# Kernel tuning notes

Measured on AMD Instinct MI355X. Metric: run time of the kernel, lower is better.

## Reference

```python
import jax, jax.numpy as jnp
import numpy as np

INV_TEMP = 20.0
THRESHOLD = 0.01
EPS = 1e-12


def setup_inputs() -> dict:
    key = jax.random.key(0)
    k1, k2, k3, k4, k5 = jax.random.split(key, 5)
    B, NA, NB, D, K = 1, 4096, 4096, 256, 8
    return {
        "keypoints_A": jax.random.uniform(k1, (B, NA, 2), jnp.float32) * 2.0 - 1.0,
        "descriptions_A": jax.random.normal(k2, (B, NA, D), jnp.float32),
        "keypoints_B": jax.random.uniform(k3, (B, NB, 2), jnp.float32) * 2.0 - 1.0,
        "descriptions_B": jax.random.normal(k4, (B, NB, D), jnp.float32),
        # steerer prototype affine maps: one DxD matrix per prototype, scaled to
        # keep steered descriptors at unit-ish norm (acts like ~orthogonal map)
        "prototype_mats": jax.random.normal(k5, (K, D, D), jnp.float32) / np.float32(np.sqrt(D)),
    }


def _neg_dist_similarity(a, b):
    # negative Euclidean distance, matching -torch.cdist(a, b)
    a2 = jnp.sum(a * a, axis=-1)[..., :, None]   # [B, NA, 1]
    b2 = jnp.sum(b * b, axis=-1)[..., None, :]   # [B, 1, NB]
    d2 = jnp.maximum(a2 + b2 - 2.0 * jnp.einsum('bnd,bmd->bnm', a, b), 0.0)
    return -jnp.sqrt(d2 + EPS)                   # [B, NA, NB]


def reference(keypoints_A, descriptions_A, keypoints_B, descriptions_B, prototype_mats):
    # base similarity
    corr = _neg_dist_similarity(descriptions_A, descriptions_B)  # [B, NA, NB]

    # looped augmented-similarity max-accumulate (one pass per prototype affine)
    def step(c, M):
        dA_aug = jnp.einsum('bnd,ed->bne', descriptions_A, M)  # steered descriptors
        return jnp.maximum(c, _neg_dist_similarity(dA_aug, descriptions_B)), None

    corr, _ = jax.lax.scan(step, corr, prototype_mats)

    corr = INV_TEMP * corr
    # dual softmax matching
    P = jax.nn.softmax(corr, axis=-2) * jax.nn.softmax(corr, axis=-1)  # [B, NA, NB]

    # mutual nearest neighbour + threshold (fixed-shape boolean mask instead of nonzero)
    mask = (P == P.max(axis=-1, keepdims=True)) \
         & (P == P.max(axis=-2, keepdims=True)) \
         & (P > THRESHOLD)

    # fixed-shape match extraction: best B-index per A keypoint + validity flag
    j = jnp.argmax(P, axis=-1)                                   # [B, NA]
    valid = jnp.take_along_axis(mask, j[..., None], axis=-1)[..., 0]  # [B, NA]
    matches_B = jnp.take_along_axis(keypoints_B, j[..., None], axis=1)  # [B, NA, 2]
    return P, mask, valid, matches_B
```

## Files before the change

### kernel.cpp

```cpp
#include <hip/hip_runtime.h>
#include <math.h>

#define NPT 4096
#define DIM 256
#define NVAR 9
#define INV_TEMP 20.0f
#define THR 0.01f
#define EPSD 1e-12f

typedef unsigned short u16;
typedef __attribute__((ext_vector_type(8))) __bf16 bf16x8;
typedef __attribute__((ext_vector_type(4))) float f32x4;

__device__ __forceinline__ unsigned frep(float x) {
    unsigned u = __float_as_uint(x);
    return (u & 0x80000000u) ? ~u : (u | 0x80000000u);
}
__device__ __forceinline__ float funrep(unsigned u) {
    return __uint_as_float((u & 0x80000000u) ? (u ^ 0x80000000u) : ~u);
}

__device__ __forceinline__ u16 f2bf(float x) {
    unsigned u = __float_as_uint(x);
    u += 0x7fffu + ((u >> 16) & 1u);
    return (u16)(u >> 16);
}
__device__ __forceinline__ float bf2f(u16 h) {
    return __uint_as_float(((unsigned)h) << 16);
}
__device__ __forceinline__ void split_hl(float x, u16& h, u16& l) {
    u16 hh = f2bf(x);
    h = hh;
    l = f2bf(x - bf2f(hh));
}

__device__ __forceinline__ void gl_lds16(const void* g, void* l) {
    __builtin_amdgcn_global_load_lds(
        (const __attribute__((address_space(1))) void*)g,
        (__attribute__((address_space(3))) void*)l, 16, 0, 0);
}

#define NA4 (NPT * DIM / 4)
#define NP4 (8 * DIM * DIM / 4)
__global__ __launch_bounds__(256) void conv3_kernel(const float* __restrict__ A,
                                                    const float* __restrict__ B,
                                                    const float* __restrict__ Pr,
                                                    u16* __restrict__ Ahi, u16* __restrict__ Alo,
                                                    u16* __restrict__ Bhi, u16* __restrict__ Blo,
                                                    u16* __restrict__ Phi, u16* __restrict__ Plo) {
    int i = blockIdx.x * 256 + threadIdx.x;
    const float* src;
    u16 *dh, *dl;
    int j;
    if (i < NA4) { src = A; dh = Ahi; dl = Alo; j = i; }
    else if (i < 2 * NA4) { src = B; dh = Bhi; dl = Blo; j = i - NA4; }
    else if (i < 2 * NA4 + NP4) { src = Pr; dh = Phi; dl = Plo; j = i - 2 * NA4; }
    else return;
    float4 v = ((const float4*)src)[j];
    ushort4 h, l;
    split_hl(v.x, h.x, l.x);
    split_hl(v.y, h.y, l.y);
    split_hl(v.z, h.z, l.z);
    split_hl(v.w, h.w, l.w);
    ((ushort4*)dh)[j] = h;
    ((ushort4*)dl)[j] = l;
}

__global__ __launch_bounds__(256, 2) void steer_mfma_kernel(
    const u16* __restrict__ A0h, const u16* __restrict__ A0l,
    const u16* __restrict__ Ph, const u16* __restrict__ Pl,
    u16* __restrict__ outH, u16* __restrict__ outL,
    float* __restrict__ a2out) {
    __shared__ u16 lds[32768];
    u16* LAh = lds;
    u16* LAl = lds + 8192;
    u16* LBh = lds + 16384;
    u16* LBl = lds + 24576;

    const int tid = threadIdx.x, lane = tid & 63, wave = tid >> 6;
    const int l15 = lane & 15, lg = lane >> 4;
    const int wr = (wave >> 1) * 64, wc = (wave & 1) * 64;
    const int rb = blockIdx.x * 128;
    const int eb = blockIdx.y * 128;
    const int k = blockIdx.z;
    const u16* Bh_g = Ph + (size_t)k * DIM * DIM;
    const u16* Bl_g = Pl + (size_t)k * DIM * DIM;
    const int s_row = tid >> 3;
    const int s_ch = tid & 7;
    const int s_gch = s_ch ^ (s_row & 7);
    const int c0 = lg ^ (l15 & 7);

    f32x4 acc[4][4];
#pragma unroll
    for (int m = 0; m < 4; ++m)
#pragma unroll
        for (int n = 0; n < 4; ++n) acc[m][n] = 0.0f;

    for (int kb = 0; kb < 4; ++kb) {
        const int k0 = kb * 64;
        __syncthreads();
#pragma unroll
        for (int r = 0; r < 4; ++r) {
            int row = r * 32 + s_row;
            size_t ga = (size_t)(rb + row) * DIM + k0 + s_gch * 8;
            size_t gb = (size_t)(eb + row) * DIM + k0 + s_gch * 8;
            int lo = row * 64 + s_ch * 8;
            gl_lds16(A0h + ga, &LAh[lo]);
            gl_lds16(A0l + ga, &LAl[lo]);
            gl_lds16(Bh_g + gb, &LBh[lo]);
            gl_lds16(Bl_g + gb, &LBl[lo]);
        }
        __syncthreads();
#pragma unroll
        for (int ks = 0; ks < 2; ++ks) {
            const int cx = (c0 ^ (ks << 2)) * 8;
            bf16x8 ah[4], al[4], bh[4], bl[4];
#pragma unroll
            for (int m = 0; m < 4; ++m) {
                int ro = (wr + m * 16 + l15) * 64 + cx;
                ah[m] = *(const bf16x8*)&LAh[ro];
                al[m] = *(const bf16x8*)&LAl[ro];
            }
#pragma unroll
            for (int n = 0; n < 4; ++n) {
                int ro = (wc + n * 16 + l15) * 64 + cx;
                bh[n] = *(const bf16x8*)&LBh[ro];
                bl[n] = *(const bf16x8*)&LBl[ro];
            }
#pragma unroll
            for (int m = 0; m < 4; ++m)
#pragma unroll
                for (int n = 0; n < 4; ++n)
                    acc[m][n] = __builtin_amdgcn_mfma_f32_16x16x32_bf16(ah[m], bh[n], acc[m][n], 0, 0, 0);
#pragma unroll
            for (int m = 0; m < 4; ++m)
#pragma unroll
                for (int n = 0; n < 4; ++n)
                    acc[m][n] = __builtin_amdgcn_mfma_f32_16x16x32_bf16(al[m], bh[n], acc[m][n], 0, 0, 0);
#pragma unroll
            for (int m = 0; m < 4; ++m)
#pragma unroll
                for (int n = 0; n < 4; ++n)
                    acc[m][n] = __builtin_amdgcn_mfma_f32_16x16x32_bf16(ah[m], bl[n], acc[m][n], 0, 0, 0);
        }
    }
#pragma unroll
    for (int m = 0; m < 4; ++m)
#pragma unroll
        for (int j = 0; j < 4; ++j) {
            size_t row = (size_t)(k + 1) * NPT + rb + wr + m * 16 + lg * 4 + j;
            float s2 = 0.f;
#pragma unroll
            for (int n = 0; n < 4; ++n) {
                float s = acc[m][n][j];
                s2 += s * s;
                u16 h, l;
                split_hl(s, h, l);
                size_t idx = row * DIM + eb + wc + n * 16 + l15;
                outH[idx] = h;
                outL[idx] = l;
            }
            s2 += __shfl_xor(s2, 1);
            s2 += __shfl_xor(s2, 2);
            s2 += __shfl_xor(s2, 4);
            s2 += __shfl_xor(s2, 8);
            if (l15 == 0) atomicAdd(&a2out[row], s2);
        }
}

__global__ __launch_bounds__(256) void rownorm2_kernel(const u16* __restrict__ AH,
                                                       const u16* __restrict__ AL,
                                                       const u16* __restrict__ BH,
                                                       const u16* __restrict__ BL,
                                                       float* __restrict__ out) {
    int w = blockIdx.x * 4 + (threadIdx.x >> 6);
    int lane = threadIdx.x & 63;
    const u16 *H, *L;
    size_t row;
    int oidx;
    if (w < NPT) { H = AH; L = AL; row = w; oidx = w; }
    else { H = BH; L = BL; row = w - NPT; oidx = NVAR * NPT + (w - NPT); }
    ushort4 h = *(const ushort4*)&H[row * DIM + lane * 4];
    ushort4 l = *(const ushort4*)&L[row * DIM + lane * 4];
    float x0 = bf2f(h.x) + bf2f(l.x);
    float x1 = bf2f(h.y) + bf2f(l.y);
    float x2 = bf2f(h.z) + bf2f(l.z);
    float x3 = bf2f(h.w) + bf2f(l.w);
    float s = x0 * x0 + x1 * x1 + x2 * x2 + x3 * x3;
#pragma unroll
    for (int o = 32; o; o >>= 1) s += __shfl_xor(s, o);
    if (lane == 0) out[oidx] = s;
}

__global__ __launch_bounds__(256, 2) void corr_mfma_kernel(
    const u16* __restrict__ Ahi, const u16* __restrict__ Alo,
    const u16* __restrict__ Bhi, const u16* __restrict__ Blo,
    const float* __restrict__ a2, const float* __restrict__ b2,
    float* __restrict__ cOut, unsigned* __restrict__ rm_rep, unsigned* __restrict__ cm_rep,
    float* __restrict__ pMaxR, float* __restrict__ pSumR,
    float* __restrict__ pMaxC, float* __restrict__ pSumC) {
    __shared__ u16 lds[32768];
    u16* LAh = lds;
    u16* LAl = lds + 8192;
    u16* LBh = lds + 16384;
    u16* LBl = lds + 24576;

    const int tid = threadIdx.x, lane = tid & 63, wave = tid >> 6;
    const int l15 = lane & 15, lg = lane >> 4;
    const int wr = (wave >> 1) * 64, wc = (wave & 1) * 64;
    int wg = blockIdx.y * 32 + blockIdx.x;
    const int xcd = wg & 7, idx8 = wg >> 3;
    const int rbIdx = ((xcd >> 1) << 3) + (idx8 >> 4);
    const int cbIdx = ((xcd & 1) << 4) + (idx8 & 15);
    const int rb = rbIdx << 7;
    const int cb = cbIdx << 7;
    const int s_row = tid >> 3;
    const int s_ch = tid & 7;
    const int s_gch = s_ch ^ (s_row & 7);
    const int c0 = lg ^ (l15 & 7);

    float b2c[4];
#pragma unroll
    for (int n = 0; n < 4; ++n) b2c[n] = b2[cb + wc + n * 16 + l15];

    f32x4 zmin[4][4];
#pragma unroll
    for (int m = 0; m < 4; ++m)
#pragma unroll
        for (int n = 0; n < 4; ++n) zmin[m][n] = 3.402823466e38f;

    for (int v = 0; v < NVAR; ++v) {
        const u16* Ah_g = Ahi + (size_t)v * NPT * DIM;
        const u16* Al_g = Alo + (size_t)v * NPT * DIM;
        f32x4 acc[4][4];
#pragma unroll
        for (int m = 0; m < 4; ++m)
#pragma unroll
            for (int n = 0; n < 4; ++n) acc[m][n] = 0.0f;

        for (int kb = 0; kb < 4; ++kb) {
            const int k0 = kb * 64;
            __syncthreads();
#pragma unroll
            for (int r = 0; r < 4; ++r) {
                int row = r * 32 + s_row;
                size_t ga = (size_t)(rb + row) * DIM + k0 + s_gch * 8;
                size_t gb = (size_t)(cb + row) * DIM + k0 + s_gch * 8;
                int lo = row * 64 + s_ch * 8;
                gl_lds16(Ah_g + ga, &LAh[lo]);
                gl_lds16(Al_g + ga, &LAl[lo]);
                gl_lds16(Bhi + gb, &LBh[lo]);
                gl_lds16(Blo + gb, &LBl[lo]);
            }
            __syncthreads();
#pragma unroll
            for (int ks = 0; ks < 2; ++ks) {
                const int cx = (c0 ^ (ks << 2)) * 8;
                bf16x8 ah[4], al[4], bh[4], bl[4];
#pragma unroll
                for (int m = 0; m < 4; ++m) {
                    int ro = (wr + m * 16 + l15) * 64 + cx;
                    ah[m] = *(const bf16x8*)&LAh[ro];
                    al[m] = *(const bf16x8*)&LAl[ro];
                }
#pragma unroll
                for (int n = 0; n < 4; ++n) {
                    int ro = (wc + n * 16 + l15) * 64 + cx;
                    bh[n] = *(const bf16x8*)&LBh[ro];
                    bl[n] = *(const bf16x8*)&LBl[ro];
                }
#pragma unroll
                for (int m = 0; m < 4; ++m)
#pragma unroll
                    for (int n = 0; n < 4; ++n)
                        acc[m][n] = __builtin_amdgcn_mfma_f32_16x16x32_bf16(ah[m], bh[n], acc[m][n], 0, 0, 0);
#pragma unroll
                for (int m = 0; m < 4; ++m)
#pragma unroll
                    for (int n = 0; n < 4; ++n)
                        acc[m][n] = __builtin_amdgcn_mfma_f32_16x16x32_bf16(al[m], bh[n], acc[m][n], 0, 0, 0);
#pragma unroll
                for (int m = 0; m < 4; ++m)
#pragma unroll
                    for (int n = 0; n < 4; ++n)
                        acc[m][n] = __builtin_amdgcn_mfma_f32_16x16x32_bf16(ah[m], bl[n], acc[m][n], 0, 0, 0);
            }
        }
#pragma unroll
        for (int m = 0; m < 4; ++m) {
            float4 a4 = *(const float4*)&a2[(size_t)v * NPT + rb + wr + m * 16 + lg * 4];
            const float* a4p = (const float*)&a4;
#pragma unroll
            for (int n = 0; n < 4; ++n)
#pragma unroll
                for (int j = 0; j < 4; ++j) {
                    float d2 = fmaxf(a4p[j] + b2c[n] - 2.0f * acc[m][n][j], 0.0f);
                    zmin[m][n][j] = fminf(zmin[m][n][j], d2);
                }
        }
    }

    unsigned* redR = (unsigned*)lds;
    unsigned* redC = redR + 128;
    float* bsumR = (float*)(redC + 128);
    float* bsumC = bsumR + 128;
    __syncthreads();
    if (tid < 128) { redR[tid] = 0u; redC[tid] = 0u; bsumR[tid] = 0.f; bsumC[tid] = 0.f; }
    __syncthreads();

    float colmax[4] = {-3.402823466e38f, -3.402823466e38f, -3.402823466e38f, -3.402823466e38f};
#pragma unroll
    for (int m = 0; m < 4; ++m) {
#pragma unroll
        for (int j = 0; j < 4; ++j) {
            int row = rb + wr + m * 16 + lg * 4 + j;
            float rmax = -3.402823466e38f;
#pragma unroll
            for (int n = 0; n < 4; ++n) {
                float c = -INV_TEMP * sqrtf(zmin[m][n][j] + EPSD);
                cOut[(size_t)row * NPT + cb + wc + n * 16 + l15] = c;
                rmax = fmaxf(rmax, c);
                colmax[n] = fmaxf(colmax[n], c);
            }
            atomicMax(&redR[wr + m * 16 + lg * 4 + j], frep(rmax));
        }
    }
#pragma unroll
    for (int n = 0; n < 4; ++n)
        atomicMax(&redC[wc + n * 16 + l15], frep(colmax[n]));
    __syncthreads();

    float bmc[4], colS[4];
#pragma unroll
    for (int n = 0; n < 4; ++n) {
        bmc[n] = funrep(redC[wc + n * 16 + l15]);
        colS[n] = 0.f;
    }
#pragma unroll
    for (int m = 0; m < 4; ++m) {
#pragma unroll
        for (int j = 0; j < 4; ++j) {
            int lr = wr + m * 16 + lg * 4 + j;
            float bm = funrep(redR[lr]);
            float s = 0.f;
#pragma unroll
            for (int n = 0; n < 4; ++n) {
                float c = -INV_TEMP * sqrtf(zmin[m][n][j] + EPSD);
                s += __expf(c - bm);
                colS[n] += __expf(c - bmc[n]);
            }
            s += __shfl_xor(s, 1);
            s += __shfl_xor(s, 2);
            s += __shfl_xor(s, 4);
            s += __shfl_xor(s, 8);
            if (l15 == 0) atomicAdd(&bsumR[lr], s);
        }
    }
#pragma unroll
    for (int n = 0; n < 4; ++n) {
        float s = colS[n];
        s += __shfl_xor(s, 16);
        s += __shfl_xor(s, 32);
        if (lg == 0) atomicAdd(&bsumC[wc + n * 16 + l15], s);
    }
    __syncthreads();

    if (tid < 128) {
        atomicMax(&rm_rep[rb + tid], redR[tid]);
        pMaxR[(size_t)cbIdx * NPT + rb + tid] = funrep(redR[tid]);
        pSumR[(size_t)cbIdx * NPT + rb + tid] = bsumR[tid];
    } else {
        int t = tid - 128;
        atomicMax(&cm_rep[cb + t], redC[t]);
        pMaxC[(size_t)rbIdx * NPT + cb + t] = funrep(redC[t]);
        pSumC[(size_t)rbIdx * NPT + cb + t] = bsumC[t];
    }
}

__global__ __launch_bounds__(256) void combine_kernel(const unsigned* __restrict__ rm_rep,
                                                      const unsigned* __restrict__ cm_rep,
                                                      const float* __restrict__ pMaxR,
                                                      const float* __restrict__ pSumR,
                                                      const float* __restrict__ pMaxC,
                                                      const float* __restrict__ pSumC,
                                                      float* __restrict__ rowsum,
                                                      float* __restrict__ colsum) {
    int idx = (blockIdx.x & 15) * 256 + threadIdx.x;
    if (blockIdx.x < 16) {
        float gm = funrep(rm_rep[idx]);
        float s = 0.f;
#pragma unroll
        for (int b = 0; b < 32; ++b)
            s += pSumR[(size_t)b * NPT + idx] * __expf(pMaxR[(size_t)b * NPT + idx] - gm);
        rowsum[idx] = s;
    } else {
        float gm = funrep(cm_rep[idx]);
        float s = 0.f;
#pragma unroll
        for (int b = 0; b < 32; ++b)
            s += pSumC[(size_t)b * NPT + idx] * __expf(pMaxC[(size_t)b * NPT + idx] - gm);
        colsum[idx] = s;
    }
}


__global__ __launch_bounds__(256) void pmax_kernel(float* __restrict__ C,
                                                   const unsigned* __restrict__ rm_rep,
                                                   const unsigned* __restrict__ cm_rep,
                                                   const float* __restrict__ rowsum,
                                                   const float* __restrict__ colsum,
                                                   unsigned* __restrict__ rmp_rep,
                                                   unsigned* __restrict__ cmp_rep) {
    const int tid = threadIdx.x, lane = tid & 63, wv = tid >> 6;
    const int c0 = (blockIdx.x & 15) * 256;
    const int r0 = (blockIdx.x >> 4) * 64;
    const int colq = (c0 >> 2) + lane;
    __shared__ float rmbuf[64], rrbuf[64];
    __shared__ float pmLds[64 * 65];
    __shared__ float qred[256];
    __shared__ float cred[4][256];
    if (tid < 64) {
        rmbuf[tid] = funrep(rm_rep[r0 + tid]);
        rrbuf[tid] = 1.0f / rowsum[r0 + tid];
    }
    uint4 cmr = ((const uint4*)cm_rep)[colq];
    float cm0 = funrep(cmr.x), cm1 = funrep(cmr.y), cm2 = funrep(cmr.z), cm3 = funrep(cmr.w);
    float4 csv = ((const float4*)colsum)[colq];
    float rc0 = 1.0f / csv.x, rc1 = 1.0f / csv.y, rc2 = 1.0f / csv.z, rc3 = 1.0f / csv.w;
    __syncthreads();
    float4 cmax = make_float4(-1.f, -1.f, -1.f, -1.f);
#pragma unroll
    for (int it = 0; it < 16; ++it) {
        int lr = it * 4 + wv;
        int r = r0 + lr;
        size_t idx = (size_t)r * (NPT / 4) + colq;
        float4 cv = ((const float4*)C)[idx];
        float rm = rmbuf[lr];
        float rr = rrbuf[lr];
        float4 p;
        p.x = __expf(2.0f * cv.x - cm0 - rm) * (rc0 * rr);
        p.y = __expf(2.0f * cv.y - cm1 - rm) * (rc1 * rr);
        p.z = __expf(2.0f * cv.z - cm2 - rm) * (rc2 * rr);
        p.w = __expf(2.0f * cv.w - cm3 - rm) * (rc3 * rr);
        ((float4*)C)[idx] = p;
        pmLds[lr * 65 + lane] = fmaxf(fmaxf(p.x, p.y), fmaxf(p.z, p.w));
        cmax.x = fmaxf(cmax.x, p.x);
        cmax.y = fmaxf(cmax.y, p.y);
        cmax.z = fmaxf(cmax.z, p.z);
        cmax.w = fmaxf(cmax.w, p.w);
    }
    cred[wv][lane * 4 + 0] = cmax.x;
    cred[wv][lane * 4 + 1] = cmax.y;
    cred[wv][lane * 4 + 2] = cmax.z;
    cred[wv][lane * 4 + 3] = cmax.w;
    __syncthreads();
    {
        int row = tid & 63, q = tid >> 6;
        float m = -1.f;
#pragma unroll
        for (int i = 0; i < 16; ++i) m = fmaxf(m, pmLds[row * 65 + q * 16 + i]);
        qred[row * 4 + q] = m;
    }
    float mc = fmaxf(fmaxf(cred[0][tid], cred[1][tid]), fmaxf(cred[2][tid], cred[3][tid]));
    atomicMax(&cmp_rep[c0 + tid], frep(mc));
    __syncthreads();
    if (tid < 64) {
        float m = fmaxf(fmaxf(qred[tid * 4 + 0], qred[tid * 4 + 1]),
                        fmaxf(qred[tid * 4 + 2], qred[tid * 4 + 3]));
        atomicMax(&rmp_rep[r0 + tid], frep(m));
    }
}

__global__ __launch_bounds__(256) void maskarg_kernel(const float* __restrict__ P,
                                                      const unsigned* __restrict__ rmp_rep,
                                                      const unsigned* __restrict__ cmp_rep,
                                                      float* __restrict__ maskOut,
                                                      int* __restrict__ argJ) {
    const int tid = threadIdx.x, lane = tid & 63, wv = tid >> 6;
    const int c0 = (blockIdx.x & 15) * 256;
    const int r0 = (blockIdx.x >> 4) * 64;
    const int colq = (c0 >> 2) + lane;
    const int col4 = c0 + lane * 4;
    __shared__ float rpbuf[64];
    __shared__ int candLds[64 * 65];
    __shared__ int qredi[256];
    if (tid < 64) rpbuf[tid] = funrep(rmp_rep[r0 + tid]);
    uint4 cpr = ((const uint4*)cmp_rep)[colq];
    float cp0 = funrep(cpr.x), cp1 = funrep(cpr.y), cp2 = funrep(cpr.z), cp3 = funrep(cpr.w);
    __syncthreads();
#pragma unroll
    for (int it = 0; it < 16; ++it) {
        int lr = it * 4 + wv;
        int r = r0 + lr;
        size_t idx = (size_t)r * (NPT / 4) + colq;
        float4 p = ((const float4*)P)[idx];
        float rmp = rpbuf[lr];
        float4 m;
        m.x = (p.x == rmp && p.x == cp0 && p.x > THR) ? 1.f : 0.f;
        m.y = (p.y == rmp && p.y == cp1 && p.y > THR) ? 1.f : 0.f;
        m.z = (p.z == rmp && p.z == cp2 && p.z > THR) ? 1.f : 0.f;
        m.w = (p.w == rmp && p.w == cp3 && p.w > THR) ? 1.f : 0.f;
        ((float4*)maskOut)[idx] = m;
        int cand = 0x7fffffff;
        if (p.w == rmp) cand = col4 + 3;
        if (p.z == rmp) cand = col4 + 2;
        if (p.y == rmp) cand = col4 + 1;
        if (p.x == rmp) cand = col4 + 0;
        candLds[lr * 65 + lane] = cand;
    }
    __syncthreads();
    {
        int row = tid & 63, q = tid >> 6;
        int m = 0x7fffffff;
#pragma unroll
        for (int i = 0; i < 16; ++i) m = min(m, candLds[row * 65 + q * 16 + i]);
        qredi[row * 4 + q] = m;
    }
    __syncthreads();
    if (tid < 64) {
        int m = min(min(qredi[tid * 4 + 0], qredi[tid * 4 + 1]),
                    min(qredi[tid * 4 + 2], qredi[tid * 4 + 3]));
        atomicMin(&argJ[r0 + tid], m);
    }
}

__global__ __launch_bounds__(256) void valid_kernel(const float* __restrict__ P,
                                                    const unsigned* __restrict__ cmp_rep,
                                                    const int* __restrict__ argJ,
                                                    const float* __restrict__ kpB,
                                                    float* __restrict__ validOut,
                                                    float* __restrict__ matchOut) {
    int n = blockIdx.x * 256 + threadIdx.x;
    int j = argJ[n];
    float pj = P[(size_t)n * NPT + j];
    bool v = (pj == funrep(cmp_rep[j])) && (pj > THR);
    validOut[n] = v ? 1.f : 0.f;
    matchOut[2 * n + 0] = kpB[2 * j + 0];
    matchOut[2 * n + 1] = kpB[2 * j + 1];
}

extern "C" void kernel_launch(void* const* d_in, const int* in_sizes, int n_in,
                              void* d_out, int out_size, void* d_ws, size_t ws_size,
                              hipStream_t stream) {
    const float* dA     = (const float*)d_in[1];
    const float* kpB    = (const float*)d_in[2];
    const float* dB     = (const float*)d_in[3];
    const float* protos = (const float*)d_in[4];

    float* P      = (float*)d_out;
    float* maskO  = P + (size_t)NPT * NPT;
    float* validO = maskO + (size_t)NPT * NPT;
    float* matchO = validO + NPT;

    u16* Ahi = (u16*)maskO;
    u16* Alo = Ahi + (size_t)NVAR * NPT * DIM;
    u16* Bhi = Alo + (size_t)NVAR * NPT * DIM;
    u16* Blo = Bhi + (size_t)NPT * DIM;
    u16* Phi = Blo + (size_t)NPT * DIM;
    u16* Plo = Phi + (size_t)8 * DIM * DIM;
    float* pMaxR = (float*)(Plo + (size_t)8 * DIM * DIM);
    float* pSumR = pMaxR + 32 * NPT;
    float* pMaxC = pSumR + 32 * NPT;
    float* pSumC = pMaxC + 32 * NPT;

    float* ws      = (float*)d_ws;
    float* a2      = ws;
    float* b2      = a2 + NVAR * NPT;
    unsigned* rm   = (unsigned*)(b2 + NPT);
    unsigned* cm   = rm + NPT;
    unsigned* rmp  = cm + NPT;
    unsigned* cmp  = rmp + NPT;
    float* rs      = (float*)(cmp + NPT);
    float* cs      = rs + NPT;
    int* argJ      = (int*)(cs + NPT);

    hipMemsetAsync(a2 + NPT, 0, 8 * NPT * sizeof(float), stream);
    hipMemsetAsync(rm, 0, 4 * NPT * sizeof(unsigned), stream);
    hipMemsetAsync(argJ, 0x7f, NPT * sizeof(int), stream);

    conv3_kernel<<<2560, 256, 0, stream>>>(dA, dB, protos, Ahi, Alo, Bhi, Blo, Phi, Plo);
    steer_mfma_kernel<<<dim3(32, 2, 8), 256, 0, stream>>>(Ahi, Alo, Phi, Plo, Ahi, Alo, a2);
    rownorm2_kernel<<<2 * NPT / 4, 256, 0, stream>>>(Ahi, Alo, Bhi, Blo, a2);
    corr_mfma_kernel<<<dim3(32, 32), 256, 0, stream>>>(Ahi, Alo, Bhi, Blo, a2, b2, P, rm, cm,
                                                       pMaxR, pSumR, pMaxC, pSumC);
    combine_kernel<<<32, 256, 0, stream>>>(rm, cm, pMaxR, pSumR, pMaxC, pSumC, rs, cs);
    pmax_kernel<<<1024, 256, 0, stream>>>(P, rm, cm, rs, cs, rmp, cmp);
    maskarg_kernel<<<1024, 256, 0, stream>>>(P, rmp, cmp, maskO, argJ);
    valid_kernel<<<16, 256, 0, stream>>>(P, cmp, argJ, kpB, validO, matchO);
}
```

Measured before the change: 424.6 us.

## Double-buffer corr GEMM LDS loads and fuse row norms into conversion

The corr kernel's K loop changes from 64-wide single-buffered tiles with two barriers per step to 32-wide double-buffered tiles. The next tile is issued into the alternate LDS buffer while MFMAs run on the current one, which hides global-load latency and leaves one barrier per step. The XOR swizzle is dropped, so LDS bank conflicts may rise. Separately, the A and B row squared norms are now computed inside the conversion kernel, which removes the rownorm2 launch and its re-read of the split data.

Measured after the change: 507.0 us. 19.4% more time.

```diff
diff --git a/kernel.cpp b/kernel.cpp
--- a/kernel.cpp
+++ b/kernel.cpp
@@ -47,13 +47,16 @@
                                                     const float* __restrict__ Pr,
                                                     u16* __restrict__ Ahi, u16* __restrict__ Alo,
                                                     u16* __restrict__ Bhi, u16* __restrict__ Blo,
-                                                    u16* __restrict__ Phi, u16* __restrict__ Plo) {
+                                                    u16* __restrict__ Phi, u16* __restrict__ Plo,
+                                                    float* __restrict__ a2,
+                                                    float* __restrict__ b2) {
     int i = blockIdx.x * 256 + threadIdx.x;
     const float* src;
     u16 *dh, *dl;
     int j;
-    if (i < NA4) { src = A; dh = Ahi; dl = Alo; j = i; }
-    else if (i < 2 * NA4) { src = B; dh = Bhi; dl = Blo; j = i - NA4; }
+    bool isA = false, isB = false;
+    if (i < NA4) { src = A; dh = Ahi; dl = Alo; j = i; isA = true; }
+    else if (i < 2 * NA4) { src = B; dh = Bhi; dl = Blo; j = i - NA4; isB = true; }
     else if (i < 2 * NA4 + NP4) { src = Pr; dh = Phi; dl = Plo; j = i - 2 * NA4; }
     else return;
     float4 v = ((const float4*)src)[j];
@@ -64,6 +67,20 @@
     split_hl(v.w, h.w, l.w);
     ((ushort4*)dh)[j] = h;
     ((ushort4*)dl)[j] = l;
+    if (isA || isB) {
+        float x0 = bf2f(h.x) + bf2f(l.x);
+        float x1 = bf2f(h.y) + bf2f(l.y);
+        float x2 = bf2f(h.z) + bf2f(l.z);
+        float x3 = bf2f(h.w) + bf2f(l.w);
+        float s = x0 * x0 + x1 * x1 + x2 * x2 + x3 * x3;
+#pragma unroll
+        for (int o = 32; o; o >>= 1) s += __shfl_xor(s, o);
+        if ((threadIdx.x & 63) == 0) {
+            int row = j >> 6;
+            if (isA) a2[row] = s;
+            else b2[row] = s;
+        }
+    }
 }
 
 __global__ __launch_bounds__(256, 2) void steer_mfma_kernel(
@@ -168,30 +185,6 @@
         }
 }
 
-__global__ __launch_bounds__(256) void rownorm2_kernel(const u16* __restrict__ AH,
-                                                       const u16* __restrict__ AL,
-                                                       const u16* __restrict__ BH,
-                                                       const u16* __restrict__ BL,
-                                                       float* __restrict__ out) {
-    int w = blockIdx.x * 4 + (threadIdx.x >> 6);
-    int lane = threadIdx.x & 63;
-    const u16 *H, *L;
-    size_t row;
-    int oidx;
-    if (w < NPT) { H = AH; L = AL; row = w; oidx = w; }
-    else { H = BH; L = BL; row = w - NPT; oidx = NVAR * NPT + (w - NPT); }
-    ushort4 h = *(const ushort4*)&H[row * DIM + lane * 4];
-    ushort4 l = *(const ushort4*)&L[row * DIM + lane * 4];
-    float x0 = bf2f(h.x) + bf2f(l.x);
-    float x1 = bf2f(h.y) + bf2f(l.y);
-    float x2 = bf2f(h.z) + bf2f(l.z);
-    float x3 = bf2f(h.w) + bf2f(l.w);
-    float s = x0 * x0 + x1 * x1 + x2 * x2 + x3 * x3;
-#pragma unroll
-    for (int o = 32; o; o >>= 1) s += __shfl_xor(s, o);
-    if (lane == 0) out[oidx] = s;
-}
-
 __global__ __launch_bounds__(256, 2) void corr_mfma_kernel(
     const u16* __restrict__ Ahi, const u16* __restrict__ Alo,
     const u16* __restrict__ Bhi, const u16* __restrict__ Blo,
@@ -200,10 +193,6 @@
     float* __restrict__ pMaxR, float* __restrict__ pSumR,
     float* __restrict__ pMaxC, float* __restrict__ pSumC) {
     __shared__ u16 lds[32768];
-    u16* LAh = lds;
-    u16* LAl = lds + 8192;
-    u16* LBh = lds + 16384;
-    u16* LBl = lds + 24576;
 
     const int tid = threadIdx.x, lane = tid & 63, wave = tid >> 6;
     const int l15 = lane & 15, lg = lane >> 4;
@@ -214,10 +203,8 @@
     const int cbIdx = ((xcd & 1) << 4) + (idx8 & 15);
     const int rb = rbIdx << 7;
     const int cb = cbIdx << 7;
-    const int s_row = tid >> 3;
-    const int s_ch = tid & 7;
-    const int s_gch = s_ch ^ (s_row & 7);
-    const int c0 = lg ^ (l15 & 7);
+    const int s_row = tid >> 2;
+    const int s_seg = (tid & 3) * 8;
 
     float b2c[4];
 #pragma unroll
@@ -229,62 +216,69 @@
 #pragma unroll
         for (int n = 0; n < 4; ++n) zmin[m][n] = 3.402823466e38f;
 
-    for (int v = 0; v < NVAR; ++v) {
+    auto STAGE = [&](int it, int buf) {
+        const int v = it >> 3, kb = it & 7, k0 = kb * 32;
         const u16* Ah_g = Ahi + (size_t)v * NPT * DIM;
         const u16* Al_g = Alo + (size_t)v * NPT * DIM;
+        u16* base = lds + buf * 16384;
+#pragma unroll
+        for (int r = 0; r < 2; ++r) {
+            int row = s_row + 64 * r;
+            size_t ga = (size_t)(rb + row) * DIM + k0 + s_seg;
+            size_t gb = (size_t)(cb + row) * DIM + k0 + s_seg;
+            int lo = row * 32 + s_seg;
+            gl_lds16(Ah_g + ga, base + lo);
+            gl_lds16(Al_g + ga, base + 4096 + lo);
+            gl_lds16(Bhi + gb, base + 8192 + lo);
+            gl_lds16(Blo + gb, base + 12288 + lo);
+        }
+    };
+
+    STAGE(0, 0);
+    __syncthreads();
+    int buf = 0;
+
+    for (int v = 0; v < NVAR; ++v) {
         f32x4 acc[4][4];
 #pragma unroll
         for (int m = 0; m < 4; ++m)
 #pragma unroll
             for (int n = 0; n < 4; ++n) acc[m][n] = 0.0f;
 
-        for (int kb = 0; kb < 4; ++kb) {
-            const int k0 = kb * 64;
+        for (int kb = 0; kb < 8; ++kb) {
+            const int it = v * 8 + kb;
+            if (it + 1 < NVAR * 8) STAGE(it + 1, buf ^ 1);
+            const u16* base = lds + buf * 16384;
+            bf16x8 ah[4], al[4], bh[4], bl[4];
+#pragma unroll
+            for (int m = 0; m < 4; ++m) {
+                int ro = (wr + m * 16 + l15) * 32 + lg * 8;
+                ah[m] = *(const bf16x8*)&base[ro];
+                al[m] = *(const bf16x8*)&base[4096 + ro];
+            }
+#pragma unroll
+            for (int n = 0; n < 4; ++n) {
+                int ro = (wc + n * 16 + l15) * 32 + lg * 8;
+                bh[n] = *(const bf16x8*)&base[8192 + ro];
+                bl[n] = *(const bf16x8*)&base[12288 + ro];
+            }
+#pragma unroll
+            for (int m = 0; m < 4; ++m)
+#pragma unroll
+                for (int n = 0; n < 4; ++n)
+                    acc[m][n] = __builtin_amdgcn_mfma_f32_16x16x32_bf16(ah[m], bh[n], acc[m][n], 0, 0, 0);
+#pragma unroll
+            for (int m = 0; m < 4; ++m)
+#pragma unroll
+                for (int n = 0; n < 4; ++n)
+                    acc[m][n] = __builtin_amdgcn_mfma_f32_16x16x32_bf16(al[m], bh[n], acc[m][n], 0, 0, 0);
+#pragma unroll
+            for (int m = 0; m < 4; ++m)
+#pragma unroll
+                for (int n = 0; n < 4; ++n)
+                    acc[m][n] = __builtin_amdgcn_mfma_f32_16x16x32_bf16(ah[m], bl[n], acc[m][n], 0, 0, 0);
             __syncthreads();
-#pragma unroll
-            for (int r = 0; r < 4; ++r) {
-                int row = r * 32 + s_row;
-                size_t ga = (size_t)(rb + row) * DIM + k0 + s_gch * 8;
-                size_t gb = (size_t)(cb + row) * DIM + k0 + s_gch * 8;
-                int lo = row * 64 + s_ch * 8;
-                gl_lds16(Ah_g + ga, &LAh[lo]);
-                gl_lds16(Al_g + ga, &LAl[lo]);
-                gl_lds16(Bhi + gb, &LBh[lo]);
-                gl_lds16(Blo + gb, &LBl[lo]);
-            }
-            __syncthreads();
-#pragma unroll
-            for (int ks = 0; ks < 2; ++ks) {
-                const int cx = (c0 ^ (ks << 2)) * 8;
-                bf16x8 ah[4], al[4], bh[4], bl[4];
-#pragma unroll
-                for (int m = 0; m < 4; ++m) {
-                    int ro = (wr + m * 16 + l15) * 64 + cx;
-                    ah[m] = *(const bf16x8*)&LAh[ro];
-                    al[m] = *(const bf16x8*)&LAl[ro];
-                }
-#pragma unroll
-                for (int n = 0; n < 4; ++n) {
-                    int ro = (wc + n * 16 + l15) * 64 + cx;
-                    bh[n] = *(const bf16x8*)&LBh[ro];
-                    bl[n] = *(const bf16x8*)&LBl[ro];
-                }
-#pragma unroll
-                for (int m = 0; m < 4; ++m)
-#pragma unroll
-                    for (int n = 0; n < 4; ++n)
-                        acc[m][n] = __builtin_amdgcn_mfma_f32_16x16x32_bf16(ah[m], bh[n], acc[m][n], 0, 0, 0);
-#pragma unroll
-                for (int m = 0; m < 4; ++m)
-#pragma unroll
-                    for (int n = 0; n < 4; ++n)
-                        acc[m][n] = __builtin_amdgcn_mfma_f32_16x16x32_bf16(al[m], bh[n], acc[m][n], 0, 0, 0);
-#pragma unroll
-                for (int m = 0; m < 4; ++m)
-#pragma unroll
-                    for (int n = 0; n < 4; ++n)
-                        acc[m][n] = __builtin_amdgcn_mfma_f32_16x16x32_bf16(ah[m], bl[n], acc[m][n], 0, 0, 0);
-            }
+            buf ^= 1;
         }
 #pragma unroll
         for (int m = 0; m < 4; ++m) {
@@ -578,9 +572,8 @@
     hipMemsetAsync(rm, 0, 4 * NPT * sizeof(unsigned), stream);
     hipMemsetAsync(argJ, 0x7f, NPT * sizeof(int), stream);
 
-    conv3_kernel<<<2560, 256, 0, stream>>>(dA, dB, protos, Ahi, Alo, Bhi, Blo, Phi, Plo);
+    conv3_kernel<<<2560, 256, 0, stream>>>(dA, dB, protos, Ahi, Alo, Bhi, Blo, Phi, Plo, a2, b2);
     steer_mfma_kernel<<<dim3(32, 2, 8), 256, 0, stream>>>(Ahi, Alo, Phi, Plo, Ahi, Alo, a2);
-    rownorm2_kernel<<<2 * NPT / 4, 256, 0, stream>>>(Ahi, Alo, Bhi, Blo, a2);
     corr_mfma_kernel<<<dim3(32, 32), 256, 0, stream>>>(Ahi, Alo, Bhi, Blo, a2, b2, P, rm, cm,
                                                        pMaxR, pSumR, pMaxC, pSumC);
     combine_kernel<<<32, 256, 0, stream>>>(rm, cm, pMaxR, pSumR, pMaxC, pSumC, rs, cs);
```

## Fold memsets, row norms and softmax-combine into neighbouring kernels

Applied to the files above, without the earlier changes.

Removes three hipMemsetAsync calls by zeroing the workspace in extra threads of the conversion kernel. Computes the base A and B row squared norms inside that same kernel with a wave reduction, dropping the separate rownorm kernel. Folds the softmax partial-sum combine into pmax_kernel, so every block recomputes its 64 row and 256 column sums from the partials. This saves launch and dependency overhead at the cost of redundant combine work, since each column sum is now recomputed by 64 blocks.

After: 414.9 us. 1.02x faster.

```diff
diff --git a/kernel.cpp b/kernel.cpp
--- a/kernel.cpp
+++ b/kernel.cpp
@@ -42,20 +42,32 @@
 
 #define NA4 (NPT * DIM / 4)
 #define NP4 (8 * DIM * DIM / 4)
+#define ZBASE (2 * NA4 + NP4)
 __global__ __launch_bounds__(256) void conv3_kernel(const float* __restrict__ A,
                                                     const float* __restrict__ B,
                                                     const float* __restrict__ Pr,
                                                     u16* __restrict__ Ahi, u16* __restrict__ Alo,
                                                     u16* __restrict__ Bhi, u16* __restrict__ Blo,
-                                                    u16* __restrict__ Phi, u16* __restrict__ Plo) {
+                                                    u16* __restrict__ Phi, u16* __restrict__ Plo,
+                                                    float* __restrict__ a2,
+                                                    float* __restrict__ b2,
+                                                    unsigned* __restrict__ zero4,
+                                                    int* __restrict__ argJ) {
     int i = blockIdx.x * 256 + threadIdx.x;
+    if (i >= ZBASE) {
+        int z = i - ZBASE;
+        if (z < 8 * NPT) a2[NPT + z] = 0.f;
+        else if (z < 12 * NPT) zero4[z - 8 * NPT] = 0u;
+        else if (z < 13 * NPT) argJ[z - 12 * NPT] = 0x7f7f7f7f;
+        return;
+    }
     const float* src;
     u16 *dh, *dl;
     int j;
-    if (i < NA4) { src = A; dh = Ahi; dl = Alo; j = i; }
-    else if (i < 2 * NA4) { src = B; dh = Bhi; dl = Blo; j = i - NA4; }
-    else if (i < 2 * NA4 + NP4) { src = Pr; dh = Phi; dl = Plo; j = i - 2 * NA4; }
-    else return;
+    bool isA = false, isB = false;
+    if (i < NA4) { src = A; dh = Ahi; dl = Alo; j = i; isA = true; }
+    else if (i < 2 * NA4) { src = B; dh = Bhi; dl = Blo; j = i - NA4; isB = true; }
+    else { src = Pr; dh = Phi; dl = Plo; j = i - 2 * NA4; }
     float4 v = ((const float4*)src)[j];
     ushort4 h, l;
     split_hl(v.x, h.x, l.x);
@@ -64,6 +76,20 @@
     split_hl(v.w, h.w, l.w);
     ((ushort4*)dh)[j] = h;
     ((ushort4*)dl)[j] = l;
+    if (isA || isB) {
+        float x0 = bf2f(h.x) + bf2f(l.x);
+        float x1 = bf2f(h.y) + bf2f(l.y);
+        float x2 = bf2f(h.z) + bf2f(l.z);
+        float x3 = bf2f(h.w) + bf2f(l.w);
+        float s = x0 * x0 + x1 * x1 + x2 * x2 + x3 * x3;
+#pragma unroll
+        for (int o = 32; o; o >>= 1) s += __shfl_xor(s, o);
+        if ((threadIdx.x & 63) == 0) {
+            int row = j >> 6;
+            if (isA) a2[row] = s;
+            else b2[row] = s;
+        }
+    }
 }
 
 __global__ __launch_bounds__(256, 2) void steer_mfma_kernel(
@@ -166,30 +192,6 @@
             s2 += __shfl_xor(s2, 8);
             if (l15 == 0) atomicAdd(&a2out[row], s2);
         }
-}
-
-__global__ __launch_bounds__(256) void rownorm2_kernel(const u16* __restrict__ AH,
-                                                       const u16* __restrict__ AL,
-                                                       const u16* __restrict__ BH,
-                                                       const u16* __restrict__ BL,
-                                                       float* __restrict__ out) {
-    int w = blockIdx.x * 4 + (threadIdx.x >> 6);
-    int lane = threadIdx.x & 63;
-    const u16 *H, *L;
-    size_t row;
-    int oidx;
-    if (w < NPT) { H = AH; L = AL; row = w; oidx = w; }
-    else { H = BH; L = BL; row = w - NPT; oidx = NVAR * NPT + (w - NPT); }
-    ushort4 h = *(const ushort4*)&H[row * DIM + lane * 4];
-    ushort4 l = *(const ushort4*)&L[row * DIM + lane * 4];
-    float x0 = bf2f(h.x) + bf2f(l.x);
-    float x1 = bf2f(h.y) + bf2f(l.y);
-    float x2 = bf2f(h.z) + bf2f(l.z);
-    float x3 = bf2f(h.w) + bf2f(l.w);
-    float s = x0 * x0 + x1 * x1 + x2 * x2 + x3 * x3;
-#pragma unroll
-    for (int o = 32; o; o >>= 1) s += __shfl_xor(s, o);
-    if (lane == 0) out[oidx] = s;
 }
 
 __global__ __launch_bounds__(256, 2) void corr_mfma_kernel(
@@ -377,38 +379,14 @@
     }
 }
 
-__global__ __launch_bounds__(256) void combine_kernel(const unsigned* __restrict__ rm_rep,
-                                                      const unsigned* __restrict__ cm_rep,
-                                                      const float* __restrict__ pMaxR,
-                                                      const float* __restrict__ pSumR,
-                                                      const float* __restrict__ pMaxC,
-                                                      const float* __restrict__ pSumC,
-                                                      float* __restrict__ rowsum,
-                                                      float* __restrict__ colsum) {
-    int idx = (blockIdx.x & 15) * 256 + threadIdx.x;
-    if (blockIdx.x < 16) {
-        float gm = funrep(rm_rep[idx]);
-        float s = 0.f;
-#pragma unroll
-        for (int b = 0; b < 32; ++b)
-            s += pSumR[(size_t)b * NPT + idx] * __expf(pMaxR[(size_t)b * NPT + idx] - gm);
-        rowsum[idx] = s;
-    } else {
-        float gm = funrep(cm_rep[idx]);
-        float s = 0.f;
-#pragma unroll
-        for (int b = 0; b < 32; ++b)
-            s += pSumC[(size_t)b * NPT + idx] * __expf(pMaxC[(size_t)b * NPT + idx] - gm);
-        colsum[idx] = s;
-    }
-}
-
 
 __global__ __launch_bounds__(256) void pmax_kernel(float* __restrict__ C,
                                                    const unsigned* __restrict__ rm_rep,
                                                    const unsigned* __restrict__ cm_rep,
-                                                   const float* __restrict__ rowsum,
-                                                   const float* __restrict__ colsum,
+                                                   const float* __restrict__ pMaxR,
+                                                   const float* __restrict__ pSumR,
+                                                   const float* __restrict__ pMaxC,
+                                                   const float* __restrict__ pSumC,
                                                    unsigned* __restrict__ rmp_rep,
                                                    unsigned* __restrict__ cmp_rep) {
     const int tid = threadIdx.x, lane = tid & 63, wv = tid >> 6;
@@ -416,18 +394,35 @@
     const int r0 = (blockIdx.x >> 4) * 64;
     const int colq = (c0 >> 2) + lane;
     __shared__ float rmbuf[64], rrbuf[64];
+    __shared__ float cmbuf[256], ccbuf[256];
     __shared__ float pmLds[64 * 65];
     __shared__ float qred[256];
     __shared__ float cred[4][256];
     if (tid < 64) {
-        rmbuf[tid] = funrep(rm_rep[r0 + tid]);
-        rrbuf[tid] = 1.0f / rowsum[r0 + tid];
-    }
-    uint4 cmr = ((const uint4*)cm_rep)[colq];
-    float cm0 = funrep(cmr.x), cm1 = funrep(cmr.y), cm2 = funrep(cmr.z), cm3 = funrep(cmr.w);
-    float4 csv = ((const float4*)colsum)[colq];
-    float rc0 = 1.0f / csv.x, rc1 = 1.0f / csv.y, rc2 = 1.0f / csv.z, rc3 = 1.0f / csv.w;
-    __syncthreads();
+        int row = r0 + tid;
+        float gm = funrep(rm_rep[row]);
+        float s = 0.f;
+#pragma unroll
+        for (int b = 0; b < 32; ++b)
+            s += pSumR[(size_t)b * NPT + row] * __expf(pMaxR[(size_t)b * NPT + row] - gm);
+        rmbuf[tid] = gm;
+        rrbuf[tid] = 1.0f / s;
+    }
+    {
+        int col = c0 + tid;
+        float gm = funrep(cm_rep[col]);
+        float s = 0.f;
+#pragma unroll
+        for (int b = 0; b < 32; ++b)
+            s += pSumC[(size_t)b * NPT + col] * __expf(pMaxC[(size_t)b * NPT + col] - gm);
+        cmbuf[tid] = gm;
+        ccbuf[tid] = 1.0f / s;
+    }
+    __syncthreads();
+    float cm0 = cmbuf[lane * 4 + 0], cm1 = cmbuf[lane * 4 + 1],
+          cm2 = cmbuf[lane * 4 + 2], cm3 = cmbuf[lane * 4 + 3];
+    float rc0 = ccbuf[lane * 4 + 0], rc1 = ccbuf[lane * 4 + 1],
+          rc2 = ccbuf[lane * 4 + 2], rc3 = ccbuf[lane * 4 + 3];
     float4 cmax = make_float4(-1.f, -1.f, -1.f, -1.f);
 #pragma unroll
     for (int it = 0; it < 16; ++it) {
@@ -570,21 +565,14 @@
     unsigned* cm   = rm + NPT;
     unsigned* rmp  = cm + NPT;
     unsigned* cmp  = rmp + NPT;
-    float* rs      = (float*)(cmp + NPT);
-    float* cs      = rs + NPT;
-    int* argJ      = (int*)(cs + NPT);
-
-    hipMemsetAsync(a2 + NPT, 0, 8 * NPT * sizeof(float), stream);
-    hipMemsetAsync(rm, 0, 4 * NPT * sizeof(unsigned), stream);
-    hipMemsetAsync(argJ, 0x7f, NPT * sizeof(int), stream);
-
-    conv3_kernel<<<2560, 256, 0, stream>>>(dA, dB, protos, Ahi, Alo, Bhi, Blo, Phi, Plo);
+    int* argJ      = (int*)(cmp + NPT);
+
+    conv3_kernel<<<2768, 256, 0, stream>>>(dA, dB, protos, Ahi, Alo, Bhi, Blo, Phi, Plo,
+                                           a2, b2, rm, argJ);
     steer_mfma_kernel<<<dim3(32, 2, 8), 256, 0, stream>>>(Ahi, Alo, Phi, Plo, Ahi, Alo, a2);
-    rownorm2_kernel<<<2 * NPT / 4, 256, 0, stream>>>(Ahi, Alo, Bhi, Blo, a2);
     corr_mfma_kernel<<<dim3(32, 32), 256, 0, stream>>>(Ahi, Alo, Bhi, Blo, a2, b2, P, rm, cm,
                                                        pMaxR, pSumR, pMaxC, pSumC);
-    combine_kernel<<<32, 256, 0, stream>>>(rm, cm, pMaxR, pSumR, pMaxC, pSumC, rs, cs);
-    pmax_kernel<<<1024, 256, 0, stream>>>(P, rm, cm, rs, cs, rmp, cmp);
+    pmax_kernel<<<1024, 256, 0, stream>>>(P, rm, cm, pMaxR, pSumR, pMaxC, pSumC, rmp, cmp);
     maskarg_kernel<<<1024, 256, 0, stream>>>(P, rmp, cmp, maskO, argJ);
     valid_kernel<<<16, 256, 0, stream>>>(P, cmp, argJ, kpB, validO, matchO);
 }
```
